# Optimization experiments

Measured on AMD Instinct MI355X. Metric: run time of the kernel, lower is better.

## Reference

```python
import jax, jax.numpy as jnp
import numpy as np

N, E, D_IN, H, OUT = 50000, 800000, 128, 256, 2
BN_EPS = 1e-5
LN_EPS = 1e-5


def _xavier(k, fi, fo):
    lim = float(np.sqrt(6.0 / (fi + fo)))
    return jax.random.uniform(k, (fi, fo), minval=-lim, maxval=lim, dtype=jnp.float32)


def setup_inputs() -> dict:
    key = jax.random.key(0)
    ks = jax.random.split(key, 8)
    return {
        "x": jax.random.normal(ks[0], (N, D_IN), dtype=jnp.float32),
        "edge_index": jax.random.randint(ks[1], (2, E), 0, N, dtype=jnp.int32),
        "feature_scale": jnp.ones((D_IN,), jnp.float32),
        "feature_bias": jnp.zeros((D_IN,), jnp.float32),
        "bn0_g": jnp.ones((D_IN,), jnp.float32),
        "bn0_b": jnp.zeros((D_IN,), jnp.float32),
        "W1": _xavier(ks[2], D_IN, H), "b1": jnp.zeros((H,), jnp.float32),
        "bn1_g": jnp.ones((H,), jnp.float32), "bn1_b": jnp.zeros((H,), jnp.float32),
        "ln1_g": jnp.ones((H,), jnp.float32), "ln1_b": jnp.zeros((H,), jnp.float32),
        "W2": _xavier(ks[3], H, H), "b2": jnp.zeros((H,), jnp.float32),
        "bn2_g": jnp.ones((H,), jnp.float32), "bn2_b": jnp.zeros((H,), jnp.float32),
        "ln2_g": jnp.ones((H,), jnp.float32), "ln2_b": jnp.zeros((H,), jnp.float32),
        "Wout": _xavier(ks[4], H, OUT), "bout": jnp.zeros((OUT,), jnp.float32),
    }


def _batchnorm(x, g, b):
    # training-mode BatchNorm1d: batch stats over node axis, biased variance
    mu = jnp.mean(x, axis=0)
    var = jnp.mean(jnp.square(x - mu), axis=0)
    return g * (x - mu) * jax.lax.rsqrt(var + BN_EPS) + b


def _layernorm(x, g, b):
    mu = jnp.mean(x, axis=-1, keepdims=True)
    var = jnp.mean(jnp.square(x - mu), axis=-1, keepdims=True)
    return g * (x - mu) * jax.lax.rsqrt(var + LN_EPS) + b


def _gcn(x, W, b, src, dst, dinv):
    # PyG GCNConv with self-loops: D^{-1/2}(A+I)D^{-1/2} X W + b
    h = x @ W                                   # [N, F]
    norm = (dinv[src] * dinv[dst])[:, None]     # [E, 1]
    msg = h[src] * norm                         # [E, F] (dominant traffic)
    agg = jax.ops.segment_sum(msg, dst, num_segments=N)
    return agg + (dinv * dinv)[:, None] * h + b


def _forward(x, feature_scale, feature_bias, bn0_g, bn0_b,
             W1, b1, bn1_g, bn1_b, ln1_g, ln1_b,
             W2, b2, bn2_g, bn2_b, ln2_g, ln2_b,
             Wout, bout, edge_index):
    src, dst = edge_index[0], edge_index[1]
    deg = jax.ops.segment_sum(jnp.ones((E,), x.dtype), dst, num_segments=N) + 1.0
    dinv = jax.lax.rsqrt(deg)

    h = x * feature_scale + feature_bias
    h = _batchnorm(h, bn0_g, bn0_b)            # input_bn; dropout = identity (eval)

    # layer 0 (no residual: i == 0)
    h1 = _gcn(h, W1, b1, src, dst, dinv)
    h1 = jax.nn.relu(h1)
    h1 = _batchnorm(h1, bn1_g, bn1_b)
    h1 = _layernorm(h1, ln1_g, ln1_b)

    # layer 1 (residual add, shapes match)
    h2 = _gcn(h1, W2, b2, src, dst, dinv)
    h2 = jax.nn.relu(h2)
    h2 = _batchnorm(h2, bn2_g, bn2_b)
    h2 = _layernorm(h2, ln2_g, ln2_b)
    h2 = h2 + h1

    return h2 @ Wout + bout


def reference(x, edge_index, feature_scale, feature_bias, bn0_g, bn0_b,
              W1, b1, bn1_g, bn1_b, ln1_g, ln1_b,
              W2, b2, bn2_g, bn2_b, ln2_g, ln2_b,
              Wout, bout):
    return _forward(x, feature_scale, feature_bias, bn0_g, bn0_b,
                    W1, b1, bn1_g, bn1_b, ln1_g, ln1_b,
                    W2, b2, bn2_g, bn2_b, ln2_g, ln2_b,
                    Wout, bout, edge_index)
```

## Files before the change

### kernel.cpp

```cpp
#include <hip/hip_runtime.h>
#include <hip/hip_bf16.h>
#include <stdint.h>

#define N_NODES 50000
#define N_EDGES 800000
#define D_IN    128
#define H_DIM   256
#define BN_EPS  1e-5f
#define LN_EPS  1e-5f
#define NBLK2 782
#define SLICE_ELEMS ((size_t)N_NODES * 32)
#define EDGE_CHUNK 3072
#define BN0_BLOCKS 256
#define PREPX_BLOCKS 6250
#define TR_BLOCKS 256
#define NBKT 196
#define CHUNK 4096
#define RCHUNKS 196

typedef float v4f __attribute__((ext_vector_type(4)));
typedef short v8s __attribute__((ext_vector_type(8)));

__device__ __forceinline__ float bflo(unsigned u){ return __uint_as_float(u << 16); }
__device__ __forceinline__ float bfhi(unsigned u){ return __uint_as_float(u & 0xffff0000u); }
__device__ __forceinline__ unsigned short f2bf(float f){
  unsigned u = __float_as_uint(f);
  u += 0x7fffu + ((u >> 16) & 1u);
  return (unsigned short)(u >> 16);
}
__device__ __forceinline__ unsigned pack2(float a, float b){
  return (unsigned)f2bf(a) | ((unsigned)f2bf(b) << 16);
}

__device__ __forceinline__ int block_excl_scan(int v){
  int t = threadIdx.x;
  int lane = t & 63, w = t >> 6;
  int inc = v;
  #pragma unroll
  for (int m = 1; m < 64; m <<= 1){
    int o = __shfl_up(inc, m, 64);
    if (lane >= m) inc += o;
  }
  __shared__ int wsum[4];
  if (lane == 63) wsum[w] = inc;
  __syncthreads();
  int base = 0;
  #pragma unroll
  for (int j = 0; j < 4; ++j) if (j < w) base += wsum[j];
  return base + inc - v;
}

__global__ __launch_bounds__(256) void bn0r1_k(const int* ei, const float* x,
                                               const float* fs, const float* fb,
                                               float* S, float* Q, int* ghist){
  int b = blockIdx.x, t = threadIdx.x;
  if (b >= BN0_BLOCKS){
    __shared__ int lh[NBKT];
    int b2 = b - BN0_BLOCKS;
    for (int i = t; i < NBKT; i += 256) lh[i] = 0;
    __syncthreads();
    int e0 = b2 * CHUNK;
    int n = min(CHUNK, N_EDGES - e0);
    for (int i = t; i < n; i += 256)
      atomicAdd(&lh[ei[N_EDGES + e0 + i] >> 8], 1);
    __syncthreads();
    if (t < NBKT && lh[t] > 0) atomicAdd(&ghist[t], lh[t]);
    return;
  }
  int cl = t & 31, rg = t >> 5;
  int c = cl * 4;
  float4 fs4 = *(const float4*)(fs + c);
  float4 fb4 = *(const float4*)(fb + c);
  float s0=0,s1=0,s2=0,s3=0,q0=0,q1=0,q2=0,q3=0;
  for (int row = b * 8 + rg; row < N_NODES; row += BN0_BLOCKS * 8){
    float4 xv = *(const float4*)(x + (size_t)row * D_IN + c);
    float v0 = xv.x * fs4.x + fb4.x;
    float v1 = xv.y * fs4.y + fb4.y;
    float v2 = xv.z * fs4.z + fb4.z;
    float v3 = xv.w * fs4.w + fb4.w;
    s0 += v0; s1 += v1; s2 += v2; s3 += v3;
    q0 += v0*v0; q1 += v1*v1; q2 += v2*v2; q3 += v3*v3;
  }
  __shared__ float red[256][8];
  red[t][0]=s0; red[t][1]=s1; red[t][2]=s2; red[t][3]=s3;
  red[t][4]=q0; red[t][5]=q1; red[t][6]=q2; red[t][7]=q3;
  __syncthreads();
  float* Sr = S + (b & 3) * D_IN;
  float* Qr = Q + (b & 3) * D_IN;
  if (t < 32){
    float a[8];
    #pragma unroll
    for (int i = 0; i < 8; ++i) a[i] = red[t][i];
    for (int j = 1; j < 8; ++j)
      #pragma unroll
      for (int i = 0; i < 8; ++i) a[i] += red[t + 32*j][i];
    #pragma unroll
    for (int i = 0; i < 4; ++i){ atomicAdd(&Sr[t*4+i], a[i]); atomicAdd(&Qr[t*4+i], a[4+i]); }
  }
}

__global__ __launch_bounds__(256) void r3_k(const int* ei, const int* ghist, int* gcursor, unsigned* ebuf){
  __shared__ unsigned short dstS[CHUNK];
  __shared__ int lh[NBKT], cb[NBKT], sbb[NBKT];
  int t = threadIdx.x;
  int v = (t < NBKT) ? ghist[t] : 0;
  int epre = block_excl_scan(v);
  if (t < NBKT){ sbb[t] = epre; lh[t] = 0; }
  __syncthreads();
  int e0 = blockIdx.x * CHUNK;
  int n = min(CHUNK, N_EDGES - e0);
  for (int i = t; i < n; i += 256){
    int d = ei[N_EDGES + e0 + i];
    dstS[i] = (unsigned short)d;
    atomicAdd(&lh[d >> 8], 1);
  }
  __syncthreads();
  if (t < NBKT && lh[t] > 0) cb[t] = sbb[t] + atomicAdd(&gcursor[t], lh[t]);
  __syncthreads();
  if (t < NBKT) lh[t] = 0;
  __syncthreads();
  for (int i = t; i < n; i += 256){
    int d = dstS[i];
    int bkt = d >> 8;
    int r = atomicAdd(&lh[bkt], 1);
    unsigned src = (unsigned)ei[e0 + i];
    ebuf[cb[bkt] + r] = ((unsigned)(d & 255) << 16) | src;
  }
}

__global__ __launch_bounds__(256) void r4a_k(const unsigned* ebuf, const int* ghist,
                                             int* cnt, int* dhist){
  __shared__ int h[256], dh[128], sbb[NBKT + 1];
  int t = threadIdx.x, b = blockIdx.x;
  int v = (t < NBKT) ? ghist[t] : 0;
  int epre = block_excl_scan(v);
  if (t < NBKT) sbb[t] = epre;
  if (t == NBKT - 1) sbb[NBKT] = epre + v;
  h[t] = 0;
  if (t < 128) dh[t] = 0;
  __syncthreads();
  int lo = sbb[b], hi = sbb[b + 1];
  for (int i = lo + t; i < hi; i += 256)
    atomicAdd(&h[(ebuf[i] >> 16) & 255], 1);
  __syncthreads();
  int node = b * 256 + t;
  if (node < N_NODES){
    cnt[node] = h[t];
    atomicAdd(&dh[min(h[t], 127)], 1);
  }
  __syncthreads();
  if (t < 128 && dh[t] > 0) atomicAdd(&dhist[t], dh[t]);
}

__global__ __launch_bounds__(256) void dperm2_k(const int* cnt, const int* dhist, int* reserve,
                                                int* perm, int* rank, int* offs, float* dinv){
  __shared__ int ep_s[128], W_s[128], lb[128], lh[128], lc[128];
  int t = threadIdx.x;
  int v = (t < 128) ? dhist[t] : 0;
  int e1 = block_excl_scan(v);
  __syncthreads();
  int e2 = block_excl_scan((t < 128) ? v * t : 0);
  __syncthreads();
  if (t < 128){ ep_s[t] = e1; W_s[t] = e2; lh[t] = 0; lc[t] = 0; }
  __syncthreads();
  for (int i = blockIdx.x * 256 + t; i < N_NODES; i += 32 * 256)
    atomicAdd(&lh[min(cnt[i], 127)], 1);
  __syncthreads();
  if (t < 128 && lh[t] > 0) lb[t] = ep_s[t] + atomicAdd(&reserve[t], lh[t]);
  __syncthreads();
  for (int i = blockIdx.x * 256 + t; i < N_NODES; i += 32 * 256){
    int d = cnt[i];
    int b = min(d, 127);
    int r = atomicAdd(&lc[b], 1);
    int pos = lb[b] + r;
    perm[pos] = i;
    rank[i] = pos;
    offs[pos] = W_s[b] + (pos - ep_s[b]) * d;
    dinv[i] = rsqrtf((float)d + 1.0f);
  }
  if (blockIdx.x == 0 && t == 0) offs[N_NODES] = N_EDGES;
}

__global__ __launch_bounds__(256) void r4bprep_k(const unsigned* ebuf, const int* ghist,
                                                 const int* rank, const int* offs,
                                                 unsigned short* edges,
                                                 const float* x, const float* S, const float* Q,
                                                 const float* fs, const float* fb,
                                                 const float* gg, const float* bb,
                                                 unsigned short* xt,
                                                 const float* W1, const float* W2,
                                                 unsigned short* W1t, unsigned short* W2t){
  __shared__ int curs[256], sbb[NBKT + 1];
  int b = blockIdx.x, t = threadIdx.x;
  if (b < NBKT){
    int v = (t < NBKT) ? ghist[t] : 0;
    int epre = block_excl_scan(v);
    if (t < NBKT) sbb[t] = epre;
    if (t == NBKT - 1) sbb[NBKT] = epre + v;
    int node = b * 256 + t;
    if (node < N_NODES) curs[t] = offs[rank[node]];
    __syncthreads();
    int lo = sbb[b], hi = sbb[b + 1];
    for (int i = lo + t; i < hi; i += 256){
      unsigned u = ebuf[i];
      int l8 = (u >> 16) & 255;
      int pos = atomicAdd(&curs[l8], 1);
      edges[pos] = (unsigned short)(u & 0xffffu);
    }
    return;
  }
  if (b < NBKT + PREPX_BLOCKS){
    int i = (b - NBKT) * 256 + t;
    int row = i >> 5; int c = (i & 31) * 4;
    float4 Sv = *(const float4*)(S + c);
    float4 Qv = *(const float4*)(Q + c);
    #pragma unroll
    for (int rep = 1; rep < 4; ++rep){
      float4 s2 = *(const float4*)(S + rep * D_IN + c);
      float4 q2 = *(const float4*)(Q + rep * D_IN + c);
      Sv.x += s2.x; Sv.y += s2.y; Sv.z += s2.z; Sv.w += s2.w;
      Qv.x += q2.x; Qv.y += q2.y; Qv.z += q2.z; Qv.w += q2.w;
    }
    float4 fs4 = *(const float4*)(fs + c);
    float4 fb4 = *(const float4*)(fb + c);
    float4 gg4 = *(const float4*)(gg + c);
    float4 bb4 = *(const float4*)(bb + c);
    const float invN = 1.0f / N_NODES;
    float mu0 = Sv.x*invN, mu1 = Sv.y*invN, mu2 = Sv.z*invN, mu3 = Sv.w*invN;
    float r0 = rsqrtf(Qv.x*invN - mu0*mu0 + BN_EPS);
    float r1 = rsqrtf(Qv.y*invN - mu1*mu1 + BN_EPS);
    float r2 = rsqrtf(Qv.z*invN - mu2*mu2 + BN_EPS);
    float r3 = rsqrtf(Qv.w*invN - mu3*mu3 + BN_EPS);
    float a0 = gg4.x*r0*fs4.x, c0 = gg4.x*r0*(fb4.x - mu0) + bb4.x;
    float a1 = gg4.y*r1*fs4.y, c1 = gg4.y*r1*(fb4.y - mu1) + bb4.y;
    float a2 = gg4.z*r2*fs4.z, c2 = gg4.z*r2*(fb4.z - mu2) + bb4.z;
    float a3 = gg4.w*r3*fs4.w, c3 = gg4.w*r3*(fb4.w - mu3) + bb4.w;
    float4 xv = *(const float4*)(x + (size_t)row * D_IN + c);
    uint2 o;
    o.x = pack2(a0 * xv.x + c0, a1 * xv.y + c1);
    o.y = pack2(a2 * xv.z + c2, a3 * xv.w + c3);
    *(uint2*)(xt + (size_t)row * D_IN + c) = o;
    return;
  }
  int i = (b - NBKT - PREPX_BLOCKS) * 256 + t;
  if (i < D_IN * H_DIM){
    int r = i / H_DIM, c = i % H_DIM;
    W1t[c * D_IN + r] = f2bf(W1[i]);
  }
  if (i < H_DIM * H_DIM){
    int r = i / H_DIM, c = i % H_DIM;
    W2t[c * H_DIM + r] = f2bf(W2[i]);
  }
}

template<int K>
__global__ __launch_bounds__(256) void gemm_k(const unsigned short* A, const unsigned short* Bt,
                                              const float* dinv, unsigned short* C, int M){
  __shared__ __align__(16) short smem[16896];
  __shared__ float dvs[64];
  short* As = smem;
  short* Bs = smem + 64 * 40;
  int t = threadIdx.x;
  int m0 = blockIdx.x * 64;
  int lane = t & 63;
  int w = t >> 6;
  int fr = lane & 15, quad = lane >> 4;
  if (t < 64) dvs[t] = (m0 + t < M) ? dinv[m0 + t] : 0.0f;
  v4f acc[4][4] = {};
  int sr = t >> 2;
  int sk = (t & 3) << 3;
  for (int k0 = 0; k0 < K; k0 += 32){
    __syncthreads();
    uint4 av = {0,0,0,0};
    int arow = m0 + sr;
    if (arow < M) av = *(const uint4*)(A + (size_t)arow * K + k0 + sk);
    *(uint4*)(&As[sr * 40 + sk]) = av;
    #pragma unroll
    for (int j = 0; j < 4; ++j){
      int brow = sr + 64 * j;
      uint4 bv = *(const uint4*)(Bt + (size_t)brow * K + k0 + sk);
      *(uint4*)(&Bs[brow * 40 + sk]) = bv;
    }
    __syncthreads();
    v8s af[4], bf[4];
    #pragma unroll
    for (int mi = 0; mi < 4; ++mi)
      af[mi] = *(const v8s*)(&As[(mi * 16 + fr) * 40 + quad * 8]);
    #pragma unroll
    for (int ni = 0; ni < 4; ++ni)
      bf[ni] = *(const v8s*)(&Bs[(w * 64 + ni * 16 + fr) * 40 + quad * 8]);
    #pragma unroll
    for (int mi = 0; mi < 4; ++mi)
      #pragma unroll
      for (int ni = 0; ni < 4; ++ni)
        acc[mi][ni] = __builtin_amdgcn_mfma_f32_16x16x32_bf16(af[mi], bf[ni], acc[mi][ni], 0, 0, 0);
  }
  __syncthreads();
  short* Cs = smem;
  #pragma unroll
  for (int mi = 0; mi < 4; ++mi)
    #pragma unroll
    for (int ni = 0; ni < 4; ++ni)
      #pragma unroll
      for (int r = 0; r < 4; ++r){
        int row = mi * 16 + quad * 4 + r;
        int col = w * 64 + ni * 16 + fr;
        Cs[row * 264 + col] = (short)f2bf(acc[mi][ni][r] * dvs[row]);
      }
  __syncthreads();
  int orow = t >> 2;
  int grow = m0 + orow;
  if (grow < M){
    #pragma unroll
    for (int j = 0; j < 4; ++j){
      int oc = (t & 3) * 16 + 64 * j;
      v8s v0 = *(const v8s*)(&Cs[orow * 264 + oc]);
      v8s v1 = *(const v8s*)(&Cs[orow * 264 + oc + 8]);
      *(v8s*)(&C[(size_t)(oc >> 5) * SLICE_ELEMS + (size_t)grow * 32 + (oc & 31)]) = v0;
      int oc1 = oc + 8;
      *(v8s*)(&C[(size_t)(oc1 >> 5) * SLICE_ELEMS + (size_t)grow * 32 + (oc1 & 31)]) = v1;
    }
  }
}

#define ACC8(vv) { a0 += bflo(vv.x); a1 += bfhi(vv.x); a2 += bflo(vv.y); a3 += bfhi(vv.y); \
                   a4 += bflo(vv.z); a5 += bfhi(vv.z); a6 += bflo(vv.w); a7 += bfhi(vv.w); }

__global__ __launch_bounds__(256) void agg_k(const unsigned short* hs, const int* offsets,
                                             const unsigned short* edges, const int* perm,
                                             const float* dinv, const float* bias,
                                             unsigned short* g, float* pS, float* pQ){
  __shared__ unsigned eds32[EDGE_CHUNK / 2];
  __shared__ float wps[4][4][16];
  int t = threadIdx.x;
  int lane = t & 63;
  int wv = t >> 6;
  int slice = blockIdx.x & 7;
  int l4 = lane & 3;
  int nb = (blockIdx.x >> 3) * 64;
  int idx = nb + (t >> 2);
  int lastn = min(nb + 64, N_NODES);
  int blk0 = offsets[nb];
  int base = blk0 & ~1;
  int blkN = offsets[lastn];
  const unsigned* gsrc = (const unsigned*)(edges + base);
  int nu = min((blkN - base + 1) >> 1, EDGE_CHUNK / 2);
  for (int i = t; i < nu; i += 256)
    eds32[i] = gsrc[i];
  __syncthreads();
  bool act = idx < N_NODES;
  int node = act ? perm[idx] : 0;
  const uint4* hb4 = (const uint4*)(hs + (size_t)slice * SLICE_ELEMS);
  float4 bb0 = *(const float4*)(bias + slice * 32 + l4 * 8);
  float4 bb1 = *(const float4*)(bias + slice * 32 + l4 * 8 + 4);
  uint4 sv = hb4[(size_t)node * 4 + l4];
  float a0 = bflo(sv.x), a1 = bfhi(sv.x);
  float a2 = bflo(sv.y), a3 = bfhi(sv.y);
  float a4 = bflo(sv.z), a5 = bfhi(sv.z);
  float a6 = bflo(sv.w), a7 = bfhi(sv.w);
  int e  = act ? offsets[idx] : 0;
  int e1 = act ? offsets[idx + 1] : 0;
  if ((e & 1) && e < e1){
    int ru = (e - base) >> 1;
    unsigned d = (ru < EDGE_CHUNK / 2) ? eds32[ru] : gsrc[ru];
    uint4 vv = hb4[(size_t)(d >> 16) * 4 + l4];
    ACC8(vv);
    ++e;
  }
  for (; e + 8 <= e1; e += 8){
    int ru = (e - base) >> 1;
    unsigned dd[4];
    if (ru + 4 <= EDGE_CHUNK / 2){
      #pragma unroll
      for (int j = 0; j < 4; ++j) dd[j] = eds32[ru + j];
    } else {
      #pragma unroll
      for (int j = 0; j < 4; ++j) dd[j] = gsrc[ru + j];
    }
    uint4 v[8];
    #pragma unroll
    for (int j = 0; j < 4; ++j){
      v[2*j]   = hb4[(size_t)(dd[j] & 0xffffu) * 4 + l4];
      v[2*j+1] = hb4[(size_t)(dd[j] >> 16)     * 4 + l4];
    }
    #pragma unroll
    for (int j = 0; j < 8; ++j) ACC8(v[j]);
  }
  if (e + 4 <= e1){
    int ru = (e - base) >> 1;
    unsigned dd[2];
    if (ru + 2 <= EDGE_CHUNK / 2){
      dd[0] = eds32[ru]; dd[1] = eds32[ru + 1];
    } else {
      dd[0] = gsrc[ru]; dd[1] = gsrc[ru + 1];
    }
    uint4 v[4];
    #pragma unroll
    for (int j = 0; j < 2; ++j){
      v[2*j]   = hb4[(size_t)(dd[j] & 0xffffu) * 4 + l4];
      v[2*j+1] = hb4[(size_t)(dd[j] >> 16)     * 4 + l4];
    }
    #pragma unroll
    for (int j = 0; j < 4; ++j) ACC8(v[j]);
    e += 4;
  }
  for (; e < e1; ++e){
    int r = e - base;
    unsigned d = ((r >> 1) < EDGE_CHUNK / 2) ? eds32[r >> 1] : gsrc[r >> 1];
    unsigned s = (r & 1) ? (d >> 16) : (d & 0xffffu);
    uint4 vv = hb4[(size_t)s * 4 + l4];
    ACC8(vv);
  }
  float dv = dinv[node];
  float y0 = act ? fmaxf(dv * a0 + bb0.x, 0.f) : 0.f;
  float y1 = act ? fmaxf(dv * a1 + bb0.y, 0.f) : 0.f;
  float y2 = act ? fmaxf(dv * a2 + bb0.z, 0.f) : 0.f;
  float y3 = act ? fmaxf(dv * a3 + bb0.w, 0.f) : 0.f;
  float y4 = act ? fmaxf(dv * a4 + bb1.x, 0.f) : 0.f;
  float y5 = act ? fmaxf(dv * a5 + bb1.y, 0.f) : 0.f;
  float y6 = act ? fmaxf(dv * a6 + bb1.z, 0.f) : 0.f;
  float y7 = act ? fmaxf(dv * a7 + bb1.w, 0.f) : 0.f;
  if (act){
    uint4 o;
    o.x = pack2(y0, y1); o.y = pack2(y2, y3);
    o.z = pack2(y4, y5); o.w = pack2(y6, y7);
    *(uint4*)(g + (size_t)node * H_DIM + slice * 32 + l4 * 8) = o;
  }
  float q0 = y0*y0, q1 = y1*y1, q2 = y2*y2, q3 = y3*y3;
  float q4 = y4*y4, q5 = y5*y5, q6 = y6*y6, q7 = y7*y7;
  #pragma unroll
  for (int m = 4; m < 64; m <<= 1){
    y0 += __shfl_xor(y0, m, 64); y1 += __shfl_xor(y1, m, 64);
    y2 += __shfl_xor(y2, m, 64); y3 += __shfl_xor(y3, m, 64);
    y4 += __shfl_xor(y4, m, 64); y5 += __shfl_xor(y5, m, 64);
    y6 += __shfl_xor(y6, m, 64); y7 += __shfl_xor(y7, m, 64);
    q0 += __shfl_xor(q0, m, 64); q1 += __shfl_xor(q1, m, 64);
    q2 += __shfl_xor(q2, m, 64); q3 += __shfl_xor(q3, m, 64);
    q4 += __shfl_xor(q4, m, 64); q5 += __shfl_xor(q5, m, 64);
    q6 += __shfl_xor(q6, m, 64); q7 += __shfl_xor(q7, m, 64);
  }
  if (lane < 4){
    wps[wv][lane][0] = y0; wps[wv][lane][1] = y1; wps[wv][lane][2] = y2; wps[wv][lane][3] = y3;
    wps[wv][lane][4] = y4; wps[wv][lane][5] = y5; wps[wv][lane][6] = y6; wps[wv][lane][7] = y7;
    wps[wv][lane][8] = q0; wps[wv][lane][9] = q1; wps[wv][lane][10] = q2; wps[wv][lane][11] = q3;
    wps[wv][lane][12] = q4; wps[wv][lane][13] = q5; wps[wv][lane][14] = q6; wps[wv][lane][15] = q7;
  }
  __syncthreads();
  if (t < 64){
    int tl = t >> 4, ti = t & 15;
    float v = wps[0][tl][ti] + wps[1][tl][ti] + wps[2][tl][ti] + wps[3][tl][ti];
    int col32 = tl * 8 + (ti & 7);
    if (ti < 8) pS[(size_t)blockIdx.x * 32 + col32] = v;
    else        pQ[(size_t)blockIdx.x * 32 + col32] = v;
  }
}

__global__ __launch_bounds__(1024) void redu_k(const float* pS, const float* pQ,
                                               const float* gg, const float* bb,
                                               float* sc, float* sh){
  __shared__ float ls[32][32], lq[32][32];
  int t = threadIdx.x;
  int slice = blockIdx.x;
  int grp = t >> 5, c32 = t & 31;
  float as = 0.f, aq = 0.f;
  for (int blk2 = grp; blk2 < NBLK2; blk2 += 32){
    size_t o = ((size_t)blk2 * 8 + slice) * 32 + c32;
    as += pS[o]; aq += pQ[o];
  }
  ls[grp][c32] = as; lq[grp][c32] = aq;
  __syncthreads();
  if (t < 32){
    float S = 0.f, Q = 0.f;
    #pragma unroll
    for (int gI = 0; gI < 32; ++gI){ S += ls[gI][t]; Q += lq[gI][t]; }
    int col = slice * 32 + t;
    const float invN = 1.0f / N_NODES;
    float mu = S * invN;
    float rs = rsqrtf(Q * invN - mu * mu + BN_EPS);
    float s = gg[col] * rs;
    sc[col] = s;
    sh[col] = bb[col] - s * mu;
  }
}

__global__ __launch_bounds__(256) void apply1_k(const unsigned short* g, const float* sc, const float* sh,
                                                const float* lng, const float* lnb, unsigned short* h1){
  int t = threadIdx.x;
  int lane32 = t & 31;
  int row = blockIdx.x * 8 + (t >> 5);
  if (row >= N_NODES) return;
  int c = lane32 * 8;
  float4 s40 = *(const float4*)(sc + c);
  float4 s41 = *(const float4*)(sc + c + 4);
  float4 h40 = *(const float4*)(sh + c);
  float4 h41 = *(const float4*)(sh + c + 4);
  uint4 u = *(const uint4*)(g + (size_t)row * H_DIM + c);
  float v0 = s40.x * bflo(u.x) + h40.x;
  float v1 = s40.y * bfhi(u.x) + h40.y;
  float v2 = s40.z * bflo(u.y) + h40.z;
  float v3 = s40.w * bfhi(u.y) + h40.w;
  float v4 = s41.x * bflo(u.z) + h41.x;
  float v5 = s41.y * bfhi(u.z) + h41.y;
  float v6 = s41.z * bflo(u.w) + h41.z;
  float v7 = s41.w * bfhi(u.w) + h41.w;
  float sum = v0+v1+v2+v3+v4+v5+v6+v7;
  float sq  = v0*v0+v1*v1+v2*v2+v3*v3+v4*v4+v5*v5+v6*v6+v7*v7;
  #pragma unroll
  for (int m = 1; m < 32; m <<= 1){ sum += __shfl_xor(sum, m, 64); sq += __shfl_xor(sq, m, 64); }
  float mu = sum * (1.0f / H_DIM);
  float var = sq * (1.0f / H_DIM) - mu * mu;
  float rs = rsqrtf(var + LN_EPS);
  float4 g40 = *(const float4*)(lng + c);
  float4 g41 = *(const float4*)(lng + c + 4);
  float4 b40 = *(const float4*)(lnb + c);
  float4 b41 = *(const float4*)(lnb + c + 4);
  uint4 o;
  o.x = pack2(g40.x * (v0 - mu) * rs + b40.x, g40.y * (v1 - mu) * rs + b40.y);
  o.y = pack2(g40.z * (v2 - mu) * rs + b40.z, g40.w * (v3 - mu) * rs + b40.w);
  o.z = pack2(g41.x * (v4 - mu) * rs + b41.x, g41.y * (v5 - mu) * rs + b41.y);
  o.w = pack2(g41.z * (v6 - mu) * rs + b41.z, g41.w * (v7 - mu) * rs + b41.w);
  *(uint4*)(h1 + (size_t)row * H_DIM + c) = o;
}

__global__ __launch_bounds__(256) void apply2_k(const unsigned short* g, const float* sc, const float* sh,
                                                const float* lng, const float* lnb,
                                                const unsigned short* h1, const float* Wout,
                                                const float* bout, float* out){
  int t = threadIdx.x;
  int lane32 = t & 31;
  int row = blockIdx.x * 8 + (t >> 5);
  if (row >= N_NODES) return;
  int c = lane32 * 8;
  float4 s40 = *(const float4*)(sc + c);
  float4 s41 = *(const float4*)(sc + c + 4);
  float4 h40 = *(const float4*)(sh + c);
  float4 h41 = *(const float4*)(sh + c + 4);
  uint4 u = *(const uint4*)(g + (size_t)row * H_DIM + c);
  float v0 = s40.x * bflo(u.x) + h40.x;
  float v1 = s40.y * bfhi(u.x) + h40.y;
  float v2 = s40.z * bflo(u.y) + h40.z;
  float v3 = s40.w * bfhi(u.y) + h40.w;
  float v4 = s41.x * bflo(u.z) + h41.x;
  float v5 = s41.y * bfhi(u.z) + h41.y;
  float v6 = s41.z * bflo(u.w) + h41.z;
  float v7 = s41.w * bfhi(u.w) + h41.w;
  float sum = v0+v1+v2+v3+v4+v5+v6+v7;
  float sq  = v0*v0+v1*v1+v2*v2+v3*v3+v4*v4+v5*v5+v6*v6+v7*v7;
  #pragma unroll
  for (int m = 1; m < 32; m <<= 1){ sum += __shfl_xor(sum, m, 64); sq += __shfl_xor(sq, m, 64); }
  float mu = sum * (1.0f / H_DIM);
  float var = sq * (1.0f / H_DIM) - mu * mu;
  float rs = rsqrtf(var + LN_EPS);
  float4 g40 = *(const float4*)(lng + c);
  float4 g41 = *(const float4*)(lng + c + 4);
  float4 b40 = *(const float4*)(lnb + c);
  float4 b41 = *(const float4*)(lnb + c + 4);
  uint4 hr = *(const uint4*)(h1 + (size_t)row * H_DIM + c);
  float y0 = g40.x * (v0 - mu) * rs + b40.x + bflo(hr.x);
  float y1 = g40.y * (v1 - mu) * rs + b40.y + bfhi(hr.x);
  float y2 = g40.z * (v2 - mu) * rs + b40.z + bflo(hr.y);
  float y3 = g40.w * (v3 - mu) * rs + b40.w + bfhi(hr.y);
  float y4 = g41.x * (v4 - mu) * rs + b41.x + bflo(hr.z);
  float y5 = g41.y * (v5 - mu) * rs + b41.y + bfhi(hr.z);
  float y6 = g41.z * (v6 - mu) * rs + b41.z + bflo(hr.w);
  float y7 = g41.w * (v7 - mu) * rs + b41.w + bfhi(hr.w);
  float4 w0 = *(const float4*)(Wout + c * 2);
  float4 w1 = *(const float4*)(Wout + c * 2 + 4);
  float4 w2 = *(const float4*)(Wout + c * 2 + 8);
  float4 w3 = *(const float4*)(Wout + c * 2 + 12);
  float o0 = y0*w0.x + y1*w0.z + y2*w1.x + y3*w1.z + y4*w2.x + y5*w2.z + y6*w3.x + y7*w3.z;
  float o1 = y0*w0.y + y1*w0.w + y2*w1.y + y3*w1.w + y4*w2.y + y5*w2.w + y6*w3.y + y7*w3.w;
  #pragma unroll
  for (int m = 1; m < 32; m <<= 1){ o0 += __shfl_xor(o0, m, 64); o1 += __shfl_xor(o1, m, 64); }
  if (lane32 == 0){
    out[(size_t)row * 2 + 0] = o0 + bout[0];
    out[(size_t)row * 2 + 1] = o1 + bout[1];
  }
}

extern "C" void kernel_launch(void* const* d_in, const int* in_sizes, int n_in,
                              void* d_out, int out_size, void* d_ws, size_t ws_size,
                              hipStream_t stream) {
  const float* x    = (const float*)d_in[0];
  const int*   ei   = (const int*)d_in[1];
  const float* fs   = (const float*)d_in[2];
  const float* fb   = (const float*)d_in[3];
  const float* bn0g = (const float*)d_in[4];
  const float* bn0b = (const float*)d_in[5];
  const float* W1   = (const float*)d_in[6];
  const float* b1   = (const float*)d_in[7];
  const float* bn1g = (const float*)d_in[8];
  const float* bn1b = (const float*)d_in[9];
  const float* ln1g = (const float*)d_in[10];
  const float* ln1b = (const float*)d_in[11];
  const float* W2   = (const float*)d_in[12];
  const float* b2   = (const float*)d_in[13];
  const float* bn2g = (const float*)d_in[14];
  const float* bn2b = (const float*)d_in[15];
  const float* ln2g = (const float*)d_in[16];
  const float* ln2b = (const float*)d_in[17];
  const float* Wout = (const float*)d_in[18];
  const float* bout = (const float*)d_in[19];
  float* out = (float*)d_out;

  char* w = (char*)d_ws;
  float* bn0S  = (float*)(w + 0);
  float* bn0Q  = (float*)(w + 2048);
  int*   dhist = (int*)(w + 4096);
  int*   reserve = (int*)(w + 4608);
  int*   ghist  = (int*)(w + 5120);
  int*   gcursor= (int*)(w + 5904);
  const size_t ZERO_BYTES = 6688;
  float* sc1   = (float*)(w + 7488);
  float* sh1   = (float*)(w + 8512);
  float* sc2   = (float*)(w + 9536);
  float* sh2   = (float*)(w + 10560);
  int*   cnt   = (int*)(w + 11584);
  float* dinv  = (float*)(w + 211584);
  int*   offs  = (int*)(w + 411584);
  int*   perm  = (int*)(w + 611712);
  int*   rank  = (int*)(w + 811712);
  unsigned short* edges = (unsigned short*)(w + 1011712);
  unsigned short* xt   = (unsigned short*)(w + 2611712);
  unsigned short* W1t  = (unsigned short*)(w + 15411712);
  unsigned short* W2t  = (unsigned short*)(w + 15477248);
  unsigned short* hlin = (unsigned short*)(w + 15608320);
  unsigned*       ebuf = (unsigned*)(w + 15608320);
  unsigned short* gbuf = (unsigned short*)(w + 41208320);
  unsigned short* h1   = (unsigned short*)(w + 66808320);
  float* pS    = (float*)(w + 92408320);
  float* pQ    = (float*)(w + 94008832);

  (void)in_sizes; (void)n_in; (void)out_size; (void)ws_size;

  hipMemsetAsync(d_ws, 0, ZERO_BYTES, stream);

  bn0r1_k<<<BN0_BLOCKS + RCHUNKS, 256, 0, stream>>>(ei, x, fs, fb, bn0S, bn0Q, ghist);
  r3_k<<<RCHUNKS, 256, 0, stream>>>(ei, ghist, gcursor, ebuf);
  r4a_k<<<NBKT, 256, 0, stream>>>(ebuf, ghist, cnt, dhist);
  dperm2_k<<<32, 256, 0, stream>>>(cnt, dhist, reserve, perm, rank, offs, dinv);
  r4bprep_k<<<NBKT + PREPX_BLOCKS + TR_BLOCKS, 256, 0, stream>>>(
      ebuf, ghist, rank, offs, edges, x, bn0S, bn0Q, fs, fb, bn0g, bn0b, xt, W1, W2, W1t, W2t);

  int ggrid = (N_NODES + 63) / 64;
  int agg_blocks = NBLK2 * 8;

  gemm_k<D_IN><<<ggrid, 256, 0, stream>>>(xt, W1t, dinv, hlin, N_NODES);
  agg_k<<<agg_blocks, 256, 0, stream>>>(hlin, offs, edges, perm, dinv, b1, gbuf, pS, pQ);
  redu_k<<<8, 1024, 0, stream>>>(pS, pQ, bn1g, bn1b, sc1, sh1);
  apply1_k<<<(N_NODES + 7) / 8, 256, 0, stream>>>(gbuf, sc1, sh1, ln1g, ln1b, h1);

  gemm_k<H_DIM><<<ggrid, 256, 0, stream>>>(h1, W2t, dinv, hlin, N_NODES);
  agg_k<<<agg_blocks, 256, 0, stream>>>(hlin, offs, edges, perm, dinv, b2, gbuf, pS, pQ);
  redu_k<<<8, 1024, 0, stream>>>(pS, pQ, bn2g, bn2b, sc2, sh2);
  apply2_k<<<(N_NODES + 7) / 8, 256, 0, stream>>>(gbuf, sc2, sh2, ln2g, ln2b, h1, Wout, bout, out);
}
```

Measured before the change: 340.5 us.

## Unroll gather loop to 16 edges, reverse block order, nontemporal output stores

The aggregation kernel now gathers 16 neighbor rows per iteration, keeping more loads in flight to hide gather latency. The edge shared-memory chunk grows, node groups are processed in reverse order (likely so heavy groups are scheduled first), the dinv load is hoisted ahead of the loop, and output stores become nontemporal. In exchange, register pressure rises, which may reduce occupancy, and the larger shared buffer uses more LDS per block.

```diff
diff --git a/kernel.cpp b/kernel.cpp
--- a/kernel.cpp
+++ b/kernel.cpp
@@ -10,7 +10,7 @@
 #define LN_EPS  1e-5f
 #define NBLK2 782
 #define SLICE_ELEMS ((size_t)N_NODES * 32)
-#define EDGE_CHUNK 3072
+#define EDGE_CHUNK 4096
 #define BN0_BLOCKS 256
 #define PREPX_BLOCKS 6250
 #define TR_BLOCKS 256
@@ -20,6 +20,7 @@
 
 typedef float v4f __attribute__((ext_vector_type(4)));
 typedef short v8s __attribute__((ext_vector_type(8)));
+typedef unsigned v4u __attribute__((ext_vector_type(4)));
 
 __device__ __forceinline__ float bflo(unsigned u){ return __uint_as_float(u << 16); }
 __device__ __forceinline__ float bfhi(unsigned u){ return __uint_as_float(u & 0xffff0000u); }
@@ -337,7 +338,8 @@
   int wv = t >> 6;
   int slice = blockIdx.x & 7;
   int l4 = lane & 3;
-  int nb = (blockIdx.x >> 3) * 64;
+  int grp = NBLK2 - 1 - (blockIdx.x >> 3);
+  int nb = grp * 64;
   int idx = nb + (t >> 2);
   int lastn = min(nb + 64, N_NODES);
   int blk0 = offsets[nb];
@@ -350,6 +352,7 @@
   __syncthreads();
   bool act = idx < N_NODES;
   int node = act ? perm[idx] : 0;
+  float dv = act ? dinv[node] : 0.f;
   const uint4* hb4 = (const uint4*)(hs + (size_t)slice * SLICE_ELEMS);
   float4 bb0 = *(const float4*)(bias + slice * 32 + l4 * 8);
   float4 bb1 = *(const float4*)(bias + slice * 32 + l4 * 8 + 4);
@@ -367,7 +370,26 @@
     ACC8(vv);
     ++e;
   }
-  for (; e + 8 <= e1; e += 8){
+  for (; e + 16 <= e1; e += 16){
+    int ru = (e - base) >> 1;
+    unsigned dd[8];
+    if (ru + 8 <= EDGE_CHUNK / 2){
+      #pragma unroll
+      for (int j = 0; j < 8; ++j) dd[j] = eds32[ru + j];
+    } else {
+      #pragma unroll
+      for (int j = 0; j < 8; ++j) dd[j] = gsrc[ru + j];
+    }
+    uint4 v[16];
+    #pragma unroll
+    for (int j = 0; j < 8; ++j){
+      v[2*j]   = hb4[(size_t)(dd[j] & 0xffffu) * 4 + l4];
+      v[2*j+1] = hb4[(size_t)(dd[j] >> 16)     * 4 + l4];
+    }
+    #pragma unroll
+    for (int j = 0; j < 16; ++j) ACC8(v[j]);
+  }
+  if (e + 8 <= e1){
     int ru = (e - base) >> 1;
     unsigned dd[4];
     if (ru + 4 <= EDGE_CHUNK / 2){
@@ -385,6 +407,7 @@
     }
     #pragma unroll
     for (int j = 0; j < 8; ++j) ACC8(v[j]);
+    e += 8;
   }
   if (e + 4 <= e1){
     int ru = (e - base) >> 1;
@@ -411,7 +434,6 @@
     uint4 vv = hb4[(size_t)s * 4 + l4];
     ACC8(vv);
   }
-  float dv = dinv[node];
   float y0 = act ? fmaxf(dv * a0 + bb0.x, 0.f) : 0.f;
   float y1 = act ? fmaxf(dv * a1 + bb0.y, 0.f) : 0.f;
   float y2 = act ? fmaxf(dv * a2 + bb0.z, 0.f) : 0.f;
@@ -421,10 +443,10 @@
   float y6 = act ? fmaxf(dv * a6 + bb1.z, 0.f) : 0.f;
   float y7 = act ? fmaxf(dv * a7 + bb1.w, 0.f) : 0.f;
   if (act){
-    uint4 o;
+    v4u o;
     o.x = pack2(y0, y1); o.y = pack2(y2, y3);
     o.z = pack2(y4, y5); o.w = pack2(y6, y7);
-    *(uint4*)(g + (size_t)node * H_DIM + slice * 32 + l4 * 8) = o;
+    __builtin_nontemporal_store(o, (v4u*)(g + (size_t)node * H_DIM + slice * 32 + l4 * 8));
   }
   float q0 = y0*y0, q1 = y1*y1, q2 = y2*y2, q3 = y3*y3;
   float q4 = y4*y4, q5 = y5*y5, q6 = y6*y6, q7 = y7*y7;
```

Result: no change. 341.4 us (+0.3%).
